# Kernel optimization log

Hardware: AMD Instinct MI355X
Metric: run time of the kernel (lower is better)

## Reference

```python
import jax, jax.numpy as jnp
import numpy as np

EPS = 1e-06


def _phi(x):
    # elu_feature_map: elu(x) + 1  (strictly positive features)
    return jax.nn.elu(x) + 1.0


def setup_inputs() -> dict:
    key = jax.random.key(0)
    k1, k2, k3 = jax.random.split(key, 3)
    N, L, H, D = 4, 4096, 12, 64
    q = jax.random.normal(k1, (N, L, H, D), dtype=jnp.float32)
    k = jax.random.normal(k2, (N, L, H, D), dtype=jnp.float32)
    v = jax.random.normal(k3, (N, L, H, D), dtype=jnp.float32)
    return {"q": q, "k": k, "v": v}


def _causal_linear_attention(q, k, v):
    qf = _phi(q)  # [N,L,H,D]
    kf = _phi(k)
    # normalizer: z_l = q_l . (sum_{s<=l} k_s) + eps
    z = jnp.einsum('nlhd,nlhd->nlh', qf, jnp.cumsum(kf, axis=1)) + EPS
    # causal_dot_product: sequential cumulative outer-product scan over L
    q_l = jnp.moveaxis(qf, 1, 0)  # [L,N,H,D]
    k_l = jnp.moveaxis(kf, 1, 0)
    v_l = jnp.moveaxis(v, 1, 0)   # [L,N,H,M]
    N, H, D = qf.shape[0], qf.shape[2], qf.shape[3]
    M = v.shape[3]
    S0 = jnp.zeros((N, H, D, M), dtype=qf.dtype)

    def step(S, qkv):
        ql, kl, vl = qkv
        S = S + jnp.einsum('nhd,nhm->nhdm', kl, vl)  # accumulate k v^T
        o = jnp.einsum('nhd,nhdm->nhm', ql, S)       # q . S
        return S, o

    _, out = jax.lax.scan(step, S0, (q_l, k_l, v_l))  # out: [L,N,H,M]
    out = jnp.moveaxis(out, 0, 1)  # [N,L,H,M]
    return out / z[..., None]


def reference(q, k, v):
    # mask=None path of LinearAttention.forward (causal linear attention)
    return _causal_linear_attention(q, k, v)
```

## Files before the change

kernel.cpp:

```cpp
#include <hip/hip_runtime.h>


#define NBATCH 4
#define LSEQ   4096
#define NHEAD  12
#define DDIM   64
#define LSTRIDE (NHEAD * DDIM)
#define NH     (NBATCH * NHEAD)
#define EPSF   1e-6f
#define CHUNK  64
#define NUMC   (LSEQ / CHUNK)
#define SB     72

typedef __attribute__((ext_vector_type(8))) short bf16x8;
typedef __attribute__((ext_vector_type(4))) float f32x4;

__device__ __forceinline__ float phi(float x) { return x > 0.f ? x + 1.f : __expf(x); }

__device__ __forceinline__ unsigned short f2bf(float x) {
    union { float f; unsigned u; } v; v.f = x;
    unsigned r = v.u + 0x7fffu + ((v.u >> 16) & 1u);
    return (unsigned short)(r >> 16);
}
__device__ __forceinline__ float bf2f(short s) {
    union { float f; unsigned u; } v; v.u = ((unsigned)(unsigned short)s) << 16;
    return v.f;
}
__device__ __forceinline__ uint2 pack4(float4 a) {
    uint2 r;
    r.x = (unsigned)f2bf(a.x) | ((unsigned)f2bf(a.y) << 16);
    r.y = (unsigned)f2bf(a.z) | ((unsigned)f2bf(a.w) << 16);
    return r;
}

__device__ __forceinline__ float4 xpose4(float4 x, int lane) {
    const bool b0 = (lane >> 4) & 1, b1 = (lane >> 5) & 1;
    float s0 = b0 ? x.x : x.y;
    float s1 = b0 ? x.z : x.w;
    s0 = __shfl_xor(s0, 16);
    s1 = __shfl_xor(s1, 16);
    float4 y;
    if (b0) { y.x = s0;  y.y = x.y; y.z = s1;  y.w = x.w; }
    else    { y.x = x.x; y.y = s0;  y.z = x.z; y.w = s1;  }
    float t0 = b1 ? y.x : y.z;
    float t1 = b1 ? y.y : y.w;
    t0 = __shfl_xor(t0, 32);
    t1 = __shfl_xor(t1, 32);
    float4 z;
    if (b1) { z.x = t0;  z.y = t1;  z.z = y.z; z.w = y.w; }
    else    { z.x = y.x; z.y = y.y; z.z = t0;  z.w = t1;  }
    return z;
}

__global__ __launch_bounds__(256) void k_sum_mf(const float* __restrict__ kin,
                                                const float* __restrict__ vin,
                                                float* __restrict__ kvws,
                                                float* __restrict__ ksws) {
    __shared__ short sKT[64 * SB];
    __shared__ short sVT[64 * SB];
    const int b = blockIdx.x, seq = b / NUMC, c = b % NUMC;
    const int n0 = seq / NHEAD, h0 = seq % NHEAD;
    const int t = threadIdx.x;
    const int gbase = ((n0 * LSEQ + c * CHUNK) * NHEAD + h0) * DDIM;
    const int lane = t & 63, w = t >> 6;
    const int nn = lane & 15, qq = lane >> 4;

#pragma unroll
    for (int rep = 0; rep < 4; ++rep) {
        const int row = rep * 16 + 4 * w + qq;
        const int c4 = nn << 2;
        const int l0 = rep * 16 + 4 * w;
        float4 kk = *(const float4*)(kin + gbase + row * LSTRIDE + c4);
        float4 kp = {phi(kk.x), phi(kk.y), phi(kk.z), phi(kk.w)};
        float4 kt = xpose4(kp, lane);
        *(uint2*)(sKT + (c4 + qq) * SB + l0) = pack4(kt);
        float4 vv = *(const float4*)(vin + gbase + row * LSTRIDE + c4);
        float4 vt = xpose4(vv, lane);
        *(uint2*)(sVT + (c4 + qq) * SB + l0) = pack4(vt);
    }
    __syncthreads();

    const int rowM = 16 * w + nn;
    bf16x8 af0 = *(const bf16x8*)(sVT + rowM * SB + qq * 8);
    bf16x8 af1 = *(const bf16x8*)(sVT + rowM * SB + 32 + qq * 8);
    float* kvb = kvws + (size_t)b * DDIM * DDIM;
    float ks = 0.f;

#pragma unroll
    for (int ct = 0; ct < 4; ++ct) {
        bf16x8 bf0 = *(const bf16x8*)(sKT + (16 * ct + nn) * SB + qq * 8);
        bf16x8 bf1 = *(const bf16x8*)(sKT + (16 * ct + nn) * SB + 32 + qq * 8);
        f32x4 acc = {0.f, 0.f, 0.f, 0.f};
        acc = __builtin_amdgcn_mfma_f32_16x16x32_bf16(af0, bf0, acc, 0, 0, 0);
        acc = __builtin_amdgcn_mfma_f32_16x16x32_bf16(af1, bf1, acc, 0, 0, 0);
        if (ct == w) {
            float s = 0.f;
#pragma unroll
            for (int j = 0; j < 8; ++j) s += bf2f(bf0[j]) + bf2f(bf1[j]);
            s += __shfl_xor(s, 16);
            s += __shfl_xor(s, 32);
            ks = s;
        }
#pragma unroll
        for (int r = 0; r < 4; ++r)
            kvb[(16 * w + 4 * qq + r) * DDIM + 16 * ct + nn] = acc[r];
    }
    if (qq == 0) ksws[b * DDIM + 16 * w + nn] = ks;
}

__global__ __launch_bounds__(64) void k_scan_mm(float* __restrict__ kv,
                                                float* __restrict__ ksum) {
    const int bid = blockIdx.x;
    const int seq = bid >> 4, part = bid & 15;
    const int t = threadIdx.x;
    float4* base = (float4*)(kv + (size_t)seq * NUMC * DDIM * DDIM) + part * 64 + t;
    float4 S = {0.f, 0.f, 0.f, 0.f};
#pragma unroll 4
    for (int c = 0; c < NUMC; ++c) {
        float4 x = base[c * (DDIM * DDIM / 4)];
        base[c * (DDIM * DDIM / 4)] = S;
        S.x += x.x; S.y += x.y; S.z += x.z; S.w += x.w;
    }
    if (part == 0) {
        float s = 0.0f;
        float* kb = ksum + (size_t)seq * NUMC * DDIM + t;
        for (int c = 0; c < NUMC; ++c) {
            float x = kb[c * DDIM];
            kb[c * DDIM] = s;
            s += x;
        }
    }
}

__global__ __launch_bounds__(256) void k_out_mf(const float* __restrict__ qin,
                                                const float* __restrict__ kin,
                                                const float* __restrict__ vin,
                                                const float* __restrict__ kvws,
                                                const float* __restrict__ ksws,
                                                float* __restrict__ out) {
    __shared__ short sQ [64 * SB];
    __shared__ short sKA[64 * SB];
    __shared__ short sVT[64 * SB];
    __shared__ short sST[64 * SB];
    __shared__ float sKs[64];
    __shared__ float sZq[64];

    const int b = blockIdx.x, seq = b / NUMC, c = b % NUMC;
    const int n0 = seq / NHEAD, h0 = seq % NHEAD;
    const int t = threadIdx.x;
    const int gbase = ((n0 * LSEQ + c * CHUNK) * NHEAD + h0) * DDIM;
    const int lane = t & 63, w = t >> 6;
    const int nn = lane & 15, qq = lane >> 4;

    if (t < 64) sKs[t] = ksws[b * DDIM + t];

    const float* Sg = kvws + (size_t)b * DDIM * DDIM;
#pragma unroll
    for (int rep = 0; rep < 4; ++rep) {
        const int row = rep * 16 + 4 * w + qq;
        const int c4 = nn << 2;
        const int l0 = rep * 16 + 4 * w;
        float4 qv = *(const float4*)(qin + gbase + row * LSTRIDE + c4);
        float4 kk = *(const float4*)(kin + gbase + row * LSTRIDE + c4);
        float4 qp = {phi(qv.x), phi(qv.y), phi(qv.z), phi(qv.w)};
        float4 kp = {phi(kk.x), phi(kk.y), phi(kk.z), phi(kk.w)};
        *(uint2*)(sQ  + row * SB + c4) = pack4(qp);
        *(uint2*)(sKA + row * SB + c4) = pack4(kp);
        float4 sv = *(const float4*)(Sg + row * 64 + c4);
        *(uint2*)(sST + row * SB + c4) = pack4(sv);
        float4 vv = *(const float4*)(vin + gbase + row * LSTRIDE + c4);
        float4 vt = xpose4(vv, lane);
        *(uint2*)(sVT + (c4 + qq) * SB + l0) = pack4(vt);
    }
    __syncthreads();

    const int rowA = 16 * w + nn;
    bf16x8 qf0 = *(const bf16x8*)(sQ + rowA * SB + qq * 8);
    bf16x8 qf1 = *(const bf16x8*)(sQ + rowA * SB + 32 + qq * 8);
    float am[4][4];
    float zrow[4] = {0.f, 0.f, 0.f, 0.f};
#pragma unroll
    for (int ct = 0; ct < 4; ++ct) {
        bf16x8 kf0 = *(const bf16x8*)(sKA + (16 * ct + nn) * SB + qq * 8);
        bf16x8 kf1 = *(const bf16x8*)(sKA + (16 * ct + nn) * SB + 32 + qq * 8);
        f32x4 acc = {0.f, 0.f, 0.f, 0.f};
        acc = __builtin_amdgcn_mfma_f32_16x16x32_bf16(qf0, kf0, acc, 0, 0, 0);
        acc = __builtin_amdgcn_mfma_f32_16x16x32_bf16(qf1, kf1, acc, 0, 0, 0);
#pragma unroll
        for (int r = 0; r < 4; ++r) {
            const int ri = 16 * w + 4 * qq + r, cj = 16 * ct + nn;
            const float mval = (cj <= ri) ? acc[r] : 0.f;
            am[ct][r] = mval;
            zrow[r] += mval;
        }
    }
#pragma unroll
    for (int r = 0; r < 4; ++r) {
        float s = zrow[r];
        s += __shfl_xor(s, 1); s += __shfl_xor(s, 2);
        s += __shfl_xor(s, 4); s += __shfl_xor(s, 8);
        zrow[r] = s;
    }
    float zq = 0.f;
#pragma unroll
    for (int j = 0; j < 8; ++j) {
        zq += bf2f(qf0[j]) * sKs[qq * 8 + j];
        zq += bf2f(qf1[j]) * sKs[32 + qq * 8 + j];
    }
    zq += __shfl_xor(zq, 16);
    zq += __shfl_xor(zq, 32);

    __syncthreads();
    if (qq == 0) sZq[16 * w + nn] = zq;
#pragma unroll
    for (int ct = 0; ct < 4; ++ct)
#pragma unroll
        for (int r = 0; r < 4; ++r)
            sKA[(16 * w + 4 * qq + r) * SB + 16 * ct + nn] = (short)f2bf(am[ct][r]);
    __syncthreads();

    f32x4 o[4] = {{0,0,0,0},{0,0,0,0},{0,0,0,0},{0,0,0,0}};
    bf16x8 af0 = *(const bf16x8*)(sKA + rowA * SB + qq * 8);
    bf16x8 af1 = *(const bf16x8*)(sKA + rowA * SB + 32 + qq * 8);
#pragma unroll
    for (int ct = 0; ct < 4; ++ct) {
        bf16x8 vf0 = *(const bf16x8*)(sVT + (16 * ct + nn) * SB + qq * 8);
        bf16x8 vf1 = *(const bf16x8*)(sVT + (16 * ct + nn) * SB + 32 + qq * 8);
        o[ct] = __builtin_amdgcn_mfma_f32_16x16x32_bf16(af0, vf0, o[ct], 0, 0, 0);
        o[ct] = __builtin_amdgcn_mfma_f32_16x16x32_bf16(af1, vf1, o[ct], 0, 0, 0);
        bf16x8 sf0 = *(const bf16x8*)(sST + (16 * ct + nn) * SB + qq * 8);
        bf16x8 sf1 = *(const bf16x8*)(sST + (16 * ct + nn) * SB + 32 + qq * 8);
        o[ct] = __builtin_amdgcn_mfma_f32_16x16x32_bf16(qf0, sf0, o[ct], 0, 0, 0);
        o[ct] = __builtin_amdgcn_mfma_f32_16x16x32_bf16(qf1, sf1, o[ct], 0, 0, 0);
    }

#pragma unroll
    for (int r = 0; r < 4; ++r) {
        const int ri = 16 * w + 4 * qq + r;
        const float z = zrow[r] + sZq[ri] + EPSF;
        const float invz = 1.f / z;
#pragma unroll
        for (int ct = 0; ct < 4; ++ct)
            out[gbase + ri * LSTRIDE + 16 * ct + nn] = o[ct][r] * invz;
    }
}

__global__ __launch_bounds__(64) void k_seq(const float* __restrict__ qin,
                                            const float* __restrict__ kin,
                                            const float* __restrict__ vin,
                                            float* __restrict__ out) {
    const int seq = blockIdx.x;
    const int n = seq / NHEAD, h = seq % NHEAD;
    const int lane = threadIdx.x;
    float Scol[DDIM];
#pragma unroll
    for (int d = 0; d < DDIM; ++d) Scol[d] = 0.0f;
    float kc = 0.0f;
    __shared__ float qk[2 * DDIM];
    int base = (n * LSEQ * NHEAD + h) * DDIM + lane;
    for (int i = 0; i < LSEQ; ++i) {
        float qval = phi(qin[base]);
        float kval = phi(kin[base]);
        float vval = vin[base];
        kc += kval;
        float zp = qval * kc;
#pragma unroll
        for (int off = 32; off > 0; off >>= 1) zp += __shfl_xor(zp, off, 64);
        float z = zp + EPSF;
        qk[2 * lane] = kval;
        qk[2 * lane + 1] = qval;
        __syncthreads();
        const float4* qk4 = (const float4*)qk;
        float acc = 0.0f;
#pragma unroll
        for (int d2 = 0; d2 < DDIM / 2; ++d2) {
            float4 t0 = qk4[d2];
            int d = 2 * d2;
            Scol[d]     += t0.x * vval;  acc += t0.y * Scol[d];
            Scol[d + 1] += t0.z * vval;  acc += t0.w * Scol[d + 1];
        }
        out[base] = acc / z;
        base += LSTRIDE;
        __syncthreads();
    }
}

extern "C" void kernel_launch(void* const* d_in, const int* in_sizes, int n_in,
                              void* d_out, int out_size, void* d_ws, size_t ws_size,
                              hipStream_t stream) {
    const float* q = (const float*)d_in[0];
    const float* k = (const float*)d_in[1];
    const float* v = (const float*)d_in[2];
    float* out = (float*)d_out;
    float* ws  = (float*)d_ws;

    const size_t need = (size_t)NH * NUMC * (DDIM * DDIM + DDIM) * sizeof(float);
    if (ws_size >= need) {
        float* kv   = ws;
        float* ksum = ws + (size_t)NH * NUMC * DDIM * DDIM;
        k_sum_mf<<<NH * NUMC, 256, 0, stream>>>(k, v, kv, ksum);
        k_scan_mm<<<NH * 16, 64, 0, stream>>>(kv, ksum);
        k_out_mf<<<NH * NUMC, 256, 0, stream>>>(q, k, v, kv, ksum, out);
    } else {
        k_seq<<<NH, 64, 0, stream>>>(q, k, v, out);
    }
}
```

Measured before the change: 224.2 us.

## Store chunk KV states in bf16 and use two-level grouped prefix scan

Per-chunk KV outer-product states are written in bf16 in MFMA-native fragment order instead of fp32, halving workspace traffic. The scan kernel now computes only group-level prefixes (every 8 chunks) from the bf16 states. Each output block rebuilds its exact prefix by adding up to 7 preceding chunk states. LDS tiles for transposed K/V use an XOR swizzle instead of padding, and launch bounds request higher occupancy. The cost is extra redundant reads and adds in the output kernel, plus extra bf16 rounding of the partial states.

```diff
diff --git a/kernel.cpp b/kernel.cpp
--- a/kernel.cpp
+++ b/kernel.cpp
@@ -10,6 +10,8 @@
 #define EPSF   1e-6f
 #define CHUNK  64
 #define NUMC   (LSEQ / CHUNK)
+#define GRP    8
+#define NGRP   (NUMC / GRP)
 #define SB     72
 
 typedef __attribute__((ext_vector_type(8))) short bf16x8;
@@ -31,6 +33,22 @@
     r.x = (unsigned)f2bf(a.x) | ((unsigned)f2bf(a.y) << 16);
     r.y = (unsigned)f2bf(a.z) | ((unsigned)f2bf(a.w) << 16);
     return r;
+}
+__device__ __forceinline__ uint2 pack4v(f32x4 a) {
+    float4 t = {a[0], a[1], a[2], a[3]};
+    return pack4(t);
+}
+__device__ __forceinline__ float4 unpack4(uint2 p) {
+    float4 a;
+    a.x = __uint_as_float(p.x << 16);
+    a.y = __uint_as_float(p.x & 0xffff0000u);
+    a.z = __uint_as_float(p.y << 16);
+    a.w = __uint_as_float(p.y & 0xffff0000u);
+    return a;
+}
+
+__device__ __forceinline__ int swz_off(int row, int u) {
+    return row * 64 + (((u ^ (row ^ (row >> 3))) & 7) << 3);
 }
 
 __device__ __forceinline__ float4 xpose4(float4 x, int lane) {
@@ -52,44 +70,49 @@
     return z;
 }
 
-__global__ __launch_bounds__(256) void k_sum_mf(const float* __restrict__ kin,
-                                                const float* __restrict__ vin,
-                                                float* __restrict__ kvws,
-                                                float* __restrict__ ksws) {
-    __shared__ short sKT[64 * SB];
-    __shared__ short sVT[64 * SB];
+__global__ __launch_bounds__(256, 4) void k_sum_mf(const float* __restrict__ kin,
+                                                   const float* __restrict__ vin,
+                                                   unsigned short* __restrict__ kv16,
+                                                   float* __restrict__ ksws) {
+    __shared__ short sKT[64 * 64];
+    __shared__ short sVT[64 * 64];
     const int b = blockIdx.x, seq = b / NUMC, c = b % NUMC;
     const int n0 = seq / NHEAD, h0 = seq % NHEAD;
     const int t = threadIdx.x;
     const int gbase = ((n0 * LSEQ + c * CHUNK) * NHEAD + h0) * DDIM;
     const int lane = t & 63, w = t >> 6;
     const int nn = lane & 15, qq = lane >> 4;
+    const int u0 = 2 * 0 + (w >> 1);
+    const int half = w & 1;
 
 #pragma unroll
     for (int rep = 0; rep < 4; ++rep) {
         const int row = rep * 16 + 4 * w + qq;
         const int c4 = nn << 2;
-        const int l0 = rep * 16 + 4 * w;
+        const int urep = 2 * rep + (w >> 1);
         float4 kk = *(const float4*)(kin + gbase + row * LSTRIDE + c4);
         float4 kp = {phi(kk.x), phi(kk.y), phi(kk.z), phi(kk.w)};
         float4 kt = xpose4(kp, lane);
-        *(uint2*)(sKT + (c4 + qq) * SB + l0) = pack4(kt);
+        const int trow = 4 * nn + qq;
+        *(uint2*)(sKT + swz_off(trow, urep) + (half << 2)) = pack4(kt);
         float4 vv = *(const float4*)(vin + gbase + row * LSTRIDE + c4);
         float4 vt = xpose4(vv, lane);
-        *(uint2*)(sVT + (c4 + qq) * SB + l0) = pack4(vt);
-    }
+        *(uint2*)(sVT + swz_off(trow, urep) + (half << 2)) = pack4(vt);
+    }
+    (void)u0;
     __syncthreads();
 
     const int rowM = 16 * w + nn;
-    bf16x8 af0 = *(const bf16x8*)(sVT + rowM * SB + qq * 8);
-    bf16x8 af1 = *(const bf16x8*)(sVT + rowM * SB + 32 + qq * 8);
-    float* kvb = kvws + (size_t)b * DDIM * DDIM;
+    bf16x8 af0 = *(const bf16x8*)(sVT + swz_off(rowM, qq));
+    bf16x8 af1 = *(const bf16x8*)(sVT + swz_off(rowM, qq + 4));
+    uint2* kvu = (uint2*)kv16 + (size_t)b * 1024;
     float ks = 0.f;
 
 #pragma unroll
     for (int ct = 0; ct < 4; ++ct) {
-        bf16x8 bf0 = *(const bf16x8*)(sKT + (16 * ct + nn) * SB + qq * 8);
-        bf16x8 bf1 = *(const bf16x8*)(sKT + (16 * ct + nn) * SB + 32 + qq * 8);
+        const int rowD = 16 * ct + nn;
+        bf16x8 bf0 = *(const bf16x8*)(sKT + swz_off(rowD, qq));
+        bf16x8 bf1 = *(const bf16x8*)(sKT + swz_off(rowD, qq + 4));
         f32x4 acc = {0.f, 0.f, 0.f, 0.f};
         acc = __builtin_amdgcn_mfma_f32_16x16x32_bf16(af0, bf0, acc, 0, 0, 0);
         acc = __builtin_amdgcn_mfma_f32_16x16x32_bf16(af1, bf1, acc, 0, 0, 0);
@@ -101,76 +124,112 @@
             s += __shfl_xor(s, 32);
             ks = s;
         }
-#pragma unroll
-        for (int r = 0; r < 4; ++r)
-            kvb[(16 * w + 4 * qq + r) * DDIM + 16 * ct + nn] = acc[r];
+        kvu[w * 256 + ct * 64 + lane] = pack4v(acc);
     }
     if (qq == 0) ksws[b * DDIM + 16 * w + nn] = ks;
 }
 
-__global__ __launch_bounds__(64) void k_scan_mm(float* __restrict__ kv,
-                                                float* __restrict__ ksum) {
+__global__ __launch_bounds__(64) void k_gscan(const unsigned short* __restrict__ kv16,
+                                              unsigned short* __restrict__ gp16,
+                                              const float* __restrict__ ksws,
+                                              float* __restrict__ gksws) {
     const int bid = blockIdx.x;
     const int seq = bid >> 4, part = bid & 15;
     const int t = threadIdx.x;
-    float4* base = (float4*)(kv + (size_t)seq * NUMC * DDIM * DDIM) + part * 64 + t;
-    float4 S = {0.f, 0.f, 0.f, 0.f};
-#pragma unroll 4
-    for (int c = 0; c < NUMC; ++c) {
-        float4 x = base[c * (DDIM * DDIM / 4)];
-        base[c * (DDIM * DDIM / 4)] = S;
-        S.x += x.x; S.y += x.y; S.z += x.z; S.w += x.w;
+    const int col = part * 64 + t;
+    const uint2* kvc = (const uint2*)kv16 + (size_t)seq * NUMC * 1024 + col;
+    uint2* gpc = (uint2*)gp16 + (size_t)seq * NGRP * 1024 + col;
+    float4 carry = {0.f, 0.f, 0.f, 0.f};
+    for (int g = 0; g < NGRP; ++g) {
+        uint2 x[GRP];
+#pragma unroll
+        for (int j = 0; j < GRP; ++j) x[j] = kvc[(g * GRP + j) * 1024];
+        gpc[g * 1024] = pack4(carry);
+#pragma unroll
+        for (int j = 0; j < GRP; ++j) {
+            float4 f = unpack4(x[j]);
+            carry.x += f.x; carry.y += f.y; carry.z += f.z; carry.w += f.w;
+        }
     }
     if (part == 0) {
-        float s = 0.0f;
-        float* kb = ksum + (size_t)seq * NUMC * DDIM + t;
-        for (int c = 0; c < NUMC; ++c) {
-            float x = kb[c * DDIM];
-            kb[c * DDIM] = s;
-            s += x;
-        }
-    }
-}
-
-__global__ __launch_bounds__(256) void k_out_mf(const float* __restrict__ qin,
-                                                const float* __restrict__ kin,
-                                                const float* __restrict__ vin,
-                                                const float* __restrict__ kvws,
-                                                const float* __restrict__ ksws,
-                                                float* __restrict__ out) {
+        float ck = 0.f;
+        const float* kc = ksws + (size_t)seq * NUMC * 64 + t;
+        float* gk = gksws + (size_t)seq * NGRP * 64 + t;
+        for (int g = 0; g < NGRP; ++g) {
+            float x[GRP];
+#pragma unroll
+            for (int j = 0; j < GRP; ++j) x[j] = kc[(g * GRP + j) * 64];
+            gk[g * 64] = ck;
+#pragma unroll
+            for (int j = 0; j < GRP; ++j) ck += x[j];
+        }
+    }
+}
+
+__global__ __launch_bounds__(256, 4) void k_out_mf(const float* __restrict__ qin,
+                                                   const float* __restrict__ kin,
+                                                   const float* __restrict__ vin,
+                                                   const unsigned short* __restrict__ kv16,
+                                                   const unsigned short* __restrict__ gp16,
+                                                   const float* __restrict__ ksws,
+                                                   const float* __restrict__ gksws,
+                                                   float* __restrict__ out) {
     __shared__ short sQ [64 * SB];
     __shared__ short sKA[64 * SB];
-    __shared__ short sVT[64 * SB];
+    __shared__ short sVT[64 * 64];
     __shared__ short sST[64 * SB];
     __shared__ float sKs[64];
     __shared__ float sZq[64];
 
     const int b = blockIdx.x, seq = b / NUMC, c = b % NUMC;
     const int n0 = seq / NHEAD, h0 = seq % NHEAD;
+    const int g = c >> 3, r8 = c & 7;
+    const int bg0 = seq * NUMC + (g << 3);
     const int t = threadIdx.x;
     const int gbase = ((n0 * LSEQ + c * CHUNK) * NHEAD + h0) * DDIM;
     const int lane = t & 63, w = t >> 6;
     const int nn = lane & 15, qq = lane >> 4;
 
-    if (t < 64) sKs[t] = ksws[b * DDIM + t];
-
-    const float* Sg = kvws + (size_t)b * DDIM * DDIM;
+    if (t < 64) {
+        float s = gksws[(seq * NGRP + g) * 64 + t];
+        for (int j = 0; j < r8; ++j) s += ksws[(bg0 + j) * 64 + t];
+        sKs[t] = s;
+    }
+
+    {
+        const uint2* kvu = (const uint2*)kv16;
+        const uint2* gpu = (const uint2*)gp16 + ((size_t)seq * NGRP + g) * 1024;
+#pragma unroll
+        for (int ct = 0; ct < 4; ++ct) {
+            const int inner = w * 256 + ct * 64 + lane;
+            float4 a = unpack4(gpu[inner]);
+            for (int j = 0; j < r8; ++j) {
+                float4 f = unpack4(kvu[(size_t)(bg0 + j) * 1024 + inner]);
+                a.x += f.x; a.y += f.y; a.z += f.z; a.w += f.w;
+            }
+            const int m0 = 16 * w + 4 * qq, dcol = 16 * ct + nn;
+            sST[(m0 + 0) * SB + dcol] = (short)f2bf(a.x);
+            sST[(m0 + 1) * SB + dcol] = (short)f2bf(a.y);
+            sST[(m0 + 2) * SB + dcol] = (short)f2bf(a.z);
+            sST[(m0 + 3) * SB + dcol] = (short)f2bf(a.w);
+        }
+    }
+
 #pragma unroll
     for (int rep = 0; rep < 4; ++rep) {
         const int row = rep * 16 + 4 * w + qq;
         const int c4 = nn << 2;
-        const int l0 = rep * 16 + 4 * w;
+        const int urep = 2 * rep + (w >> 1);
+        const int half = w & 1;
         float4 qv = *(const float4*)(qin + gbase + row * LSTRIDE + c4);
         float4 kk = *(const float4*)(kin + gbase + row * LSTRIDE + c4);
         float4 qp = {phi(qv.x), phi(qv.y), phi(qv.z), phi(qv.w)};
         float4 kp = {phi(kk.x), phi(kk.y), phi(kk.z), phi(kk.w)};
         *(uint2*)(sQ  + row * SB + c4) = pack4(qp);
         *(uint2*)(sKA + row * SB + c4) = pack4(kp);
-        float4 sv = *(const float4*)(Sg + row * 64 + c4);
-        *(uint2*)(sST + row * SB + c4) = pack4(sv);
         float4 vv = *(const float4*)(vin + gbase + row * LSTRIDE + c4);
         float4 vt = xpose4(vv, lane);
-        *(uint2*)(sVT + (c4 + qq) * SB + l0) = pack4(vt);
+        *(uint2*)(sVT + swz_off(4 * nn + qq, urep) + (half << 2)) = pack4(vt);
     }
     __syncthreads();
 
@@ -224,12 +283,13 @@
     bf16x8 af1 = *(const bf16x8*)(sKA + rowA * SB + 32 + qq * 8);
 #pragma unroll
     for (int ct = 0; ct < 4; ++ct) {
-        bf16x8 vf0 = *(const bf16x8*)(sVT + (16 * ct + nn) * SB + qq * 8);
-        bf16x8 vf1 = *(const bf16x8*)(sVT + (16 * ct + nn) * SB + 32 + qq * 8);
+        const int rowT = 16 * ct + nn;
+        bf16x8 vf0 = *(const bf16x8*)(sVT + swz_off(rowT, qq));
+        bf16x8 vf1 = *(const bf16x8*)(sVT + swz_off(rowT, qq + 4));
         o[ct] = __builtin_amdgcn_mfma_f32_16x16x32_bf16(af0, vf0, o[ct], 0, 0, 0);
         o[ct] = __builtin_amdgcn_mfma_f32_16x16x32_bf16(af1, vf1, o[ct], 0, 0, 0);
-        bf16x8 sf0 = *(const bf16x8*)(sST + (16 * ct + nn) * SB + qq * 8);
-        bf16x8 sf1 = *(const bf16x8*)(sST + (16 * ct + nn) * SB + 32 + qq * 8);
+        bf16x8 sf0 = *(const bf16x8*)(sST + rowT * SB + qq * 8);
+        bf16x8 sf1 = *(const bf16x8*)(sST + rowT * SB + 32 + qq * 8);
         o[ct] = __builtin_amdgcn_mfma_f32_16x16x32_bf16(qf0, sf0, o[ct], 0, 0, 0);
         o[ct] = __builtin_amdgcn_mfma_f32_16x16x32_bf16(qf1, sf1, o[ct], 0, 0, 0);
     }
@@ -292,15 +352,21 @@
     const float* k = (const float*)d_in[1];
     const float* v = (const float*)d_in[2];
     float* out = (float*)d_out;
-    float* ws  = (float*)d_ws;
-
-    const size_t need = (size_t)NH * NUMC * (DDIM * DDIM + DDIM) * sizeof(float);
+
+    const size_t kv_shorts = (size_t)NH * NUMC * 4096;
+    const size_t gp_shorts = (size_t)NH * NGRP * 4096;
+    const size_t ks_floats = (size_t)NH * NUMC * 64;
+    const size_t gk_floats = (size_t)NH * NGRP * 64;
+    const size_t need = (kv_shorts + gp_shorts) * 2 + (ks_floats + gk_floats) * 4;
+
     if (ws_size >= need) {
-        float* kv   = ws;
-        float* ksum = ws + (size_t)NH * NUMC * DDIM * DDIM;
-        k_sum_mf<<<NH * NUMC, 256, 0, stream>>>(k, v, kv, ksum);
-        k_scan_mm<<<NH * 16, 64, 0, stream>>>(kv, ksum);
-        k_out_mf<<<NH * NUMC, 256, 0, stream>>>(q, k, v, kv, ksum, out);
+        unsigned short* kv16 = (unsigned short*)d_ws;
+        unsigned short* gp16 = kv16 + kv_shorts;
+        float* ksum  = (float*)(gp16 + gp_shorts);
+        float* gksum = ksum + ks_floats;
+        k_sum_mf<<<NH * NUMC, 256, 0, stream>>>(k, v, kv16, ksum);
+        k_gscan<<<NH * 16, 64, 0, stream>>>(kv16, gp16, ksum, gksum);
+        k_out_mf<<<NH * NUMC, 256, 0, stream>>>(q, k, v, kv16, gp16, ksum, gksum, out);
     } else {
         k_seq<<<NH, 64, 0, stream>>>(q, k, v, out);
     }
```

Result: slower. 241.6 us (+7.8%).
